# Optimization experiments

Measured on AMD Instinct MI355X. Metric: run time of the kernel, lower is better.

## Reference

```python
import jax, jax.numpy as jnp
import numpy as np

B, N, E, C, ND, MID, OUT = 4, 16384, 131072, 128, 3, 128, 128


def setup_inputs() -> dict:
    key = jax.random.key(0)
    ks = jax.random.split(key, 11)
    f = jax.random.normal(ks[0], (B, C, N), dtype=jnp.float32)
    nodes = jax.random.normal(ks[1], (B, N, ND), dtype=jnp.float32)
    node_weights = jax.random.uniform(ks[2], (B, N, 1), dtype=jnp.float32)  # positive quadrature weights
    edges_index = jax.random.randint(ks[3], (B, E, 2), 0, N)
    edge_gradient_weights = jax.random.normal(ks[4], (B, E, ND), dtype=jnp.float32) * 0.1
    mlp_w1 = jax.random.normal(ks[5], (MID, ND * C), dtype=jnp.float32) * 0.02
    mlp_b1 = jnp.zeros((MID,), dtype=jnp.float32)
    mlp_w2 = jax.random.normal(ks[6], (OUT, MID), dtype=jnp.float32) * 0.02
    mlp_b2 = jnp.zeros((OUT,), dtype=jnp.float32)
    L = jax.random.normal(ks[7], (ND, ND), dtype=jnp.float32) * 0.1  # Cholesky factor (scaled for non-degenerate exp)
    chol_bias = jnp.zeros((ND,), dtype=jnp.float32)
    return dict(f=f, nodes=nodes, node_weights=node_weights, edges_index=edges_index,
                edge_gradient_weights=edge_gradient_weights, mlp_w1=mlp_w1, mlp_b1=mlp_b1,
                mlp_w2=mlp_w2, mlp_b2=mlp_b2, L=L, chol_bias=chol_bias)


def reference(f, nodes, node_weights, edges_index, edge_gradient_weights,
              mlp_w1, mlp_b1, mlp_w2, mlp_b2, L, chol_bias):
    b, c, n = f.shape
    nd = edge_gradient_weights.shape[-1]
    bidx = jnp.arange(b)[:, None]
    src_g = edges_index[..., 0]
    tgt_g = edges_index[..., 1]

    # ---- compute_gradient: gather f[src]-f[tgt], weight by edge_gradient_weights, scatter-add to target ----
    fT = f.transpose(0, 2, 1)  # (B,N,C)
    df = jnp.take_along_axis(fT, src_g[..., None], axis=1) - jnp.take_along_axis(fT, tgt_g[..., None], axis=1)  # (B,E,C)
    msg = (df[:, :, :, None] * edge_gradient_weights[:, :, None, :]).reshape(b, df.shape[1], c * nd)  # 'bed,bec->becd'
    grad = jnp.zeros((b, n, c * nd), f.dtype).at[bidx, tgt_g].add(msg)
    g = grad.transpose(0, 2, 1)  # (B, C*nd, N)

    # ---- pointwise MLP over channel dim (Conv1d k=1 -> GELU -> Conv1d k=1) ----
    h = jnp.einsum('mk,bkn->bmn', mlp_w1, g) + mlp_b1[None, :, None]
    h = jax.nn.gelu(h, approximate=False)
    h = jnp.einsum('om,bmn->bon', mlp_w2, h) + mlp_b2[None, :, None]
    fo = h.transpose(0, 2, 1)  # (B,N,OUT)
    o = fo.shape[-1]

    # ---- Gaussian edge kernel via Cholesky PSD form, with self-edges appended ----
    self_e = jnp.broadcast_to(jnp.arange(n)[None, :], (b, n))
    src = jnp.concatenate([src_g, self_e], axis=-1)
    tgt = jnp.concatenate([tgt_g, self_e], axis=-1)
    f_src = jnp.take_along_axis(fo, src[..., None], axis=1)  # (B,E+N,OUT)
    d = jnp.take_along_axis(nodes, src[..., None], axis=1) - jnp.take_along_axis(nodes, tgt[..., None], axis=1)  # (B,E+N,nd)
    Sigma = L @ L.T  # positive semi-definite inverse covariance
    dS = d @ Sigma.T + chol_bias  # F.linear
    w_src = jnp.take_along_axis(node_weights, src[..., None], axis=1)[..., 0]  # (B,E+N)
    kernel = w_src * jnp.exp(-jnp.einsum('bed,bed->be', d, dS))

    # ---- scatter-add normalization and aggregation ----
    inv = 1.0 / jnp.zeros((b, n), f.dtype).at[bidx, tgt].add(kernel)
    out = jnp.zeros((b, n, o), f.dtype).at[bidx, tgt].add(f_src * kernel[..., None]) * inv[..., None]
    return out.transpose(0, 2, 1)  # (B,OUT,N)
```

## Files before the change

### kernel.cpp

```cpp
#include <hip/hip_runtime.h>
#include <hip/hip_bf16.h>

static constexpr int B   = 4;
static constexpr int N   = 16384;
static constexpr int E   = 131072;
static constexpr int C   = 128;
static constexpr int ND  = 3;
static constexpr int MID = 128;
static constexpr int OUT = 128;
static constexpr int K1  = C * ND;
static constexpr int NT  = 32;
static constexpr int K1P = 392;

typedef __attribute__((ext_vector_type(8))) short bf16x8;
typedef __attribute__((ext_vector_type(4))) float f32x4;

__device__ __forceinline__ ushort f2bf(float x) {
    union { float f; unsigned u; } v; v.f = x;
    return (ushort)((v.u + 0x7fffu + ((v.u >> 16) & 1u)) >> 16);
}
__device__ __forceinline__ float bf2f(ushort u) {
    union { unsigned u; float f; } v; v.u = (unsigned)u << 16;
    return v.f;
}

__global__ void k_prep(const float* __restrict__ W1, const float* __restrict__ W2,
                       const float* __restrict__ L, ushort* __restrict__ W1p,
                       ushort* __restrict__ W2p, float* __restrict__ Sig) {
    int gid = blockIdx.x * 256 + threadIdx.x;
    for (int i = gid; i < 8 * 12 * 64 * 8; i += 64 * 256) {
        int j = i & 7, l = (i >> 3) & 63, t = (i >> 9) % 12, nt = (i >> 9) / 12;
        int n = nt * 16 + (l & 15);
        int k = t * 32 + ((l >> 4) & 3) * 8 + j;
        W1p[i] = f2bf(W1[n * K1 + k]);
    }
    for (int i = gid; i < 8 * 4 * 64 * 8; i += 64 * 256) {
        int j = i & 7, l = (i >> 3) & 63, t = (i >> 9) % 4, nt = (i >> 9) / 4;
        int n = nt * 16 + (l & 15);
        int k = t * 32 + ((l >> 4) & 3) * 8 + j;
        W2p[i] = f2bf(W2[n * MID + k]);
    }
    if (gid < 9) {
        int i = gid / 3, j = gid % 3;
        Sig[gid] = L[i * 3 + 0] * L[j * 3 + 0] + L[i * 3 + 1] * L[j * 3 + 1] +
                   L[i * 3 + 2] * L[j * 3 + 2];
    }
}

__global__ void k_transpose(const float* __restrict__ f, ushort* __restrict__ fT) {
    __shared__ float tile[32][33];
    int b = blockIdx.z;
    int n0 = blockIdx.x * 32, c0 = blockIdx.y * 32;
    const float* fb = f + (size_t)b * C * N;
    ushort* fTb = fT + (size_t)b * N * C;
    int tx = threadIdx.x, ty = threadIdx.y;
    #pragma unroll
    for (int i = 0; i < 32; i += 8)
        tile[ty + i][tx] = fb[(size_t)(c0 + ty + i) * N + n0 + tx];
    __syncthreads();
    #pragma unroll
    for (int i = 0; i < 32; i += 8)
        fTb[(size_t)(n0 + ty + i) * C + c0 + tx] = f2bf(tile[tx][ty + i]);
}

__global__ void k_count(const int2* __restrict__ ei2, int* __restrict__ deg) {
    int idx = blockIdx.x * 256 + threadIdx.x;
    int b = idx >> 17;
    int tgt = ei2[idx].y;
    atomicAdd(&deg[b * N + tgt], 1);
}

__global__ void k_scan1(const int4* __restrict__ degv, int* __restrict__ rowptr,
                        int* __restrict__ bsum) {
    __shared__ int s[256];
    int blk = blockIdx.x, t = threadIdx.x;
    int4 d = degv[blk * 256 + t];
    s[t] = d.x + d.y + d.z + d.w;
    __syncthreads();
    for (int off = 1; off < 256; off <<= 1) {
        int v = s[t];
        int u = (t >= off) ? s[t - off] : 0;
        __syncthreads();
        s[t] = v + u;
        __syncthreads();
    }
    int excl = (t == 0) ? 0 : s[t - 1];
    if (t == 255) bsum[blk] = s[255];
    int4 w;
    w.x = excl;
    w.y = excl + d.x;
    w.z = w.y + d.y;
    w.w = w.z + d.z;
    ((int4*)rowptr)[blk * 256 + t] = w;
}

__global__ void k_scan2(int* __restrict__ bsum, int* __restrict__ rowptr) {
    __shared__ int s[64];
    int t = threadIdx.x;
    s[t] = bsum[t];
    __syncthreads();
    for (int off = 1; off < 64; off <<= 1) {
        int v = s[t];
        int u = (t >= off) ? s[t - off] : 0;
        __syncthreads();
        s[t] = v + u;
        __syncthreads();
    }
    bsum[t] = (t == 0) ? 0 : s[t - 1];
    if (t == 63) rowptr[B * N] = s[63];
}

__global__ void k_scan3(int4* __restrict__ rowv, const int* __restrict__ bsum) {
    int i = blockIdx.x * 256 + threadIdx.x;
    int add = bsum[i >> 8];
    int4 v = rowv[i];
    v.x += add; v.y += add; v.z += add; v.w += add;
    rowv[i] = v;
}

__global__ void k_fill_perm(const int2* __restrict__ ei2,
                            const int* __restrict__ rowptr,
                            int* __restrict__ cursor, int* __restrict__ perm) {
    int idx = blockIdx.x * 256 + threadIdx.x;
    int b = idx >> 17;
    int tgt = ei2[idx].y;
    int bn = b * N + tgt;
    int pos = atomicAdd(&cursor[bn], 1);
    perm[rowptr[bn] + pos] = idx;
}

__global__ void k_fill_expand(const int* __restrict__ perm,
                              const int2* __restrict__ ei2,
                              const float* __restrict__ egw,
                              const float* __restrict__ nodes,
                              const float* __restrict__ nw,
                              const float* __restrict__ Sig,
                              const float* __restrict__ cb,
                              float4* __restrict__ egwp, float2* __restrict__ ka2) {
    int o = blockIdx.x * 256 + threadIdx.x;
    int idx = perm[o];
    int b = idx >> 17;
    int2 e = ei2[idx];
    int src = e.x, tgt = e.y;
    const float* w = egw + (size_t)idx * ND;
    egwp[o] = make_float4(w[0], w[1], w[2], __int_as_float(src));
    const float* ns = nodes + ((size_t)b * N + src) * ND;
    const float* nt = nodes + ((size_t)b * N + tgt) * ND;
    float d0 = ns[0] - nt[0], d1 = ns[1] - nt[1], d2 = ns[2] - nt[2];
    float q = d0 * (Sig[0] * d0 + Sig[1] * d1 + Sig[2] * d2) +
              d1 * (Sig[3] * d0 + Sig[4] * d1 + Sig[5] * d2) +
              d2 * (Sig[6] * d0 + Sig[7] * d1 + Sig[8] * d2) +
              d0 * cb[0] + d1 * cb[1] + d2 * cb[2];
    ka2[o] = make_float2(nw[(size_t)b * N + src] * expf(-q), __int_as_float(src));
}

#define EDGE_FMA(W, U)                                                         \
    {                                                                          \
        float dx = bf2f(U.x) - ft.x, dy = bf2f(U.y) - ft.y,                    \
              dz = bf2f(U.z) - ft.z, dw = bf2f(U.w) - ft.w;                    \
        a0.x = fmaf(dx, W.x, a0.x); a0.y = fmaf(dy, W.x, a0.y);                \
        a0.z = fmaf(dz, W.x, a0.z); a0.w = fmaf(dw, W.x, a0.w);                \
        a1.x = fmaf(dx, W.y, a1.x); a1.y = fmaf(dy, W.y, a1.y);                \
        a1.z = fmaf(dz, W.y, a1.z); a1.w = fmaf(dw, W.y, a1.w);                \
        a2.x = fmaf(dx, W.z, a2.x); a2.y = fmaf(dy, W.z, a2.y);                \
        a2.z = fmaf(dz, W.z, a2.z); a2.w = fmaf(dw, W.z, a2.w);                \
    }

__global__ __launch_bounds__(512, 5) void k_grad_mlp(
    const ushort* __restrict__ fT, const int* __restrict__ rowptr,
    const float4* __restrict__ egwp, const ushort* __restrict__ W1p,
    const float* __restrict__ b1, const ushort* __restrict__ W2p,
    const float* __restrict__ b2, ushort* __restrict__ fo) {
    __shared__ ushort g_s[NT][K1P];
    int tid = threadIdx.x;
    int n0 = blockIdx.x * NT;

    {
        int cg = tid & 31, s = tid >> 5;
        int cg4 = cg * 4;
        for (int jj = 0; jj < NT; jj += 16) {
            int j = jj + s;
            int n = n0 + j;
            const ushort* fTb = fT + (size_t)(n >> 14) * N * C;
            float4 ft;
            {
                ushort4 u = *(const ushort4*)(fT + (size_t)n * C + cg4);
                ft = make_float4(bf2f(u.x), bf2f(u.y), bf2f(u.z), bf2f(u.w));
            }
            int base = rowptr[n], cnt = rowptr[n + 1] - base;
            float4 a0 = make_float4(0.f, 0.f, 0.f, 0.f), a1 = a0, a2 = a0;
            int i = 0;
            for (; i + 4 <= cnt; i += 4) {
                float4 w0 = egwp[base + i];
                float4 w1 = egwp[base + i + 1];
                float4 w2 = egwp[base + i + 2];
                float4 w3 = egwp[base + i + 3];
                ushort4 u0 = *(const ushort4*)(fTb + (size_t)__float_as_int(w0.w) * C + cg4);
                ushort4 u1 = *(const ushort4*)(fTb + (size_t)__float_as_int(w1.w) * C + cg4);
                ushort4 u2 = *(const ushort4*)(fTb + (size_t)__float_as_int(w2.w) * C + cg4);
                ushort4 u3 = *(const ushort4*)(fTb + (size_t)__float_as_int(w3.w) * C + cg4);
                EDGE_FMA(w0, u0);
                EDGE_FMA(w1, u1);
                EDGE_FMA(w2, u2);
                EDGE_FMA(w3, u3);
            }
            for (; i < cnt; ++i) {
                float4 w0 = egwp[base + i];
                ushort4 u0 = *(const ushort4*)(fTb + (size_t)__float_as_int(w0.w) * C + cg4);
                EDGE_FMA(w0, u0);
            }
            unsigned p0 = (unsigned)f2bf(a0.x) | ((unsigned)f2bf(a1.x) << 16);
            unsigned p1 = (unsigned)f2bf(a2.x) | ((unsigned)f2bf(a0.y) << 16);
            unsigned p2 = (unsigned)f2bf(a1.y) | ((unsigned)f2bf(a2.y) << 16);
            unsigned p3 = (unsigned)f2bf(a0.z) | ((unsigned)f2bf(a1.z) << 16);
            unsigned p4 = (unsigned)f2bf(a2.z) | ((unsigned)f2bf(a0.w) << 16);
            unsigned p5 = (unsigned)f2bf(a1.w) | ((unsigned)f2bf(a2.w) << 16);
            uint2* dst = (uint2*)&g_s[j][cg * 12];
            dst[0] = make_uint2(p0, p1);
            dst[1] = make_uint2(p2, p3);
            dst[2] = make_uint2(p4, p5);
        }
    }
    __syncthreads();

    int wv = tid >> 6, ln = tid & 63, lr = ln & 15, lh = ln >> 4;
    int mt = wv & 1, nh = wv >> 1;
    bf16x8 a[12];
    {
        const ushort* grow = &g_s[mt * 16 + lr][0];
        #pragma unroll
        for (int t = 0; t < 12; ++t)
            a[t] = *(const bf16x8*)(grow + t * 32 + lh * 8);
    }
    __syncthreads();

    ushort(*h_s)[136] = (ushort(*)[136]) & g_s[0][0];
    const bf16x8* W1f = (const bf16x8*)W1p;
    #pragma unroll
    for (int q = 0; q < 2; ++q) {
        int nt = nh * 2 + q;
        float bb = b1[nt * 16 + lr];
        f32x4 c = {bb, bb, bb, bb};
        #pragma unroll
        for (int t = 0; t < 12; ++t)
            c = __builtin_amdgcn_mfma_f32_16x16x32_bf16(
                a[t], W1f[(nt * 12 + t) * 64 + ln], c, 0, 0, 0);
        #pragma unroll
        for (int r = 0; r < 4; ++r) {
            float x = c[r];
            x = 0.5f * x * (1.0f + erff(x * 0.70710678118654752f));
            h_s[mt * 16 + lh * 4 + r][nt * 16 + lr] = f2bf(x);
        }
    }
    __syncthreads();

    bf16x8 a2[4];
    {
        const ushort* hrow = &h_s[mt * 16 + lr][0];
        #pragma unroll
        for (int t = 0; t < 4; ++t)
            a2[t] = *(const bf16x8*)(hrow + t * 32 + lh * 8);
    }
    const bf16x8* W2f = (const bf16x8*)W2p;
    #pragma unroll
    for (int q = 0; q < 2; ++q) {
        int nt = nh * 2 + q;
        float bb = b2[nt * 16 + lr];
        f32x4 c = {bb, bb, bb, bb};
        #pragma unroll
        for (int t = 0; t < 4; ++t)
            c = __builtin_amdgcn_mfma_f32_16x16x32_bf16(
                a2[t], W2f[(nt * 4 + t) * 64 + ln], c, 0, 0, 0);
        #pragma unroll
        for (int r = 0; r < 4; ++r)
            fo[(size_t)(n0 + mt * 16 + lh * 4 + r) * OUT + nt * 16 + lr] = f2bf(c[r]);
    }
}

#define AGG_FMA(K, U)                                                          \
    {                                                                          \
        o.x = fmaf(bf2f(U.x), K.x, o.x); o.y = fmaf(bf2f(U.y), K.x, o.y);      \
        o.z = fmaf(bf2f(U.z), K.x, o.z); o.w = fmaf(bf2f(U.w), K.x, o.w);      \
        den += K.x;                                                            \
    }

__global__ __launch_bounds__(512, 5) void k_agg_t(const ushort* __restrict__ fo,
                                                  const float* __restrict__ nw,
                                                  const int* __restrict__ rowptr,
                                                  const float2* __restrict__ ka2,
                                                  float* __restrict__ out) {
    __shared__ float t[OUT][65];
    int tid = threadIdx.x;
    int cg4 = (tid & 31) * 4;
    int s = tid >> 5;
    int n0 = blockIdx.x * 64;
    int b = n0 >> 14, ncol0 = n0 & (N - 1);
    const ushort* fob = fo + (size_t)b * N * OUT;
    for (int g = 0; g < 4; ++g) {
        int nl = g * 16 + s;
        int n = n0 + nl;
        int base = rowptr[n], cnt = rowptr[n + 1] - base;
        float4 o = make_float4(0.f, 0.f, 0.f, 0.f);
        float den = 0.f;
        int i = 0;
        for (; i + 4 <= cnt; i += 4) {
            float2 k0 = ka2[base + i];
            float2 k1 = ka2[base + i + 1];
            float2 k2 = ka2[base + i + 2];
            float2 k3 = ka2[base + i + 3];
            ushort4 u0 = *(const ushort4*)(fob + (size_t)__float_as_int(k0.y) * OUT + cg4);
            ushort4 u1 = *(const ushort4*)(fob + (size_t)__float_as_int(k1.y) * OUT + cg4);
            ushort4 u2 = *(const ushort4*)(fob + (size_t)__float_as_int(k2.y) * OUT + cg4);
            ushort4 u3 = *(const ushort4*)(fob + (size_t)__float_as_int(k3.y) * OUT + cg4);
            AGG_FMA(k0, u0);
            AGG_FMA(k1, u1);
            AGG_FMA(k2, u2);
            AGG_FMA(k3, u3);
        }
        for (; i < cnt; ++i) {
            float2 k0 = ka2[base + i];
            ushort4 u0 = *(const ushort4*)(fob + (size_t)__float_as_int(k0.y) * OUT + cg4);
            AGG_FMA(k0, u0);
        }
        float wn = nw[n];
        ushort4 uf = *(const ushort4*)(fo + (size_t)n * OUT + cg4);
        float inv = 1.f / (den + wn);
        t[cg4 + 0][nl] = (o.x + bf2f(uf.x) * wn) * inv;
        t[cg4 + 1][nl] = (o.y + bf2f(uf.y) * wn) * inv;
        t[cg4 + 2][nl] = (o.z + bf2f(uf.z) * wn) * inv;
        t[cg4 + 3][nl] = (o.w + bf2f(uf.w) * wn) * inv;
    }
    __syncthreads();
    #pragma unroll
    for (int i = 0; i < 16; ++i) {
        int idx = tid + i * 512;
        int o = idx >> 6, nl = idx & 63;
        out[((size_t)b * OUT + o) * N + ncol0 + nl] = t[o][nl];
    }
}

extern "C" void kernel_launch(void* const* d_in, const int* in_sizes, int n_in,
                              void* d_out, int out_size, void* d_ws, size_t ws_size,
                              hipStream_t stream) {
    const float* f     = (const float*)d_in[0];
    const float* nodes = (const float*)d_in[1];
    const float* nw    = (const float*)d_in[2];
    const int*   ei    = (const int*)d_in[3];
    const float* egw   = (const float*)d_in[4];
    const float* W1    = (const float*)d_in[5];
    const float* b1    = (const float*)d_in[6];
    const float* W2    = (const float*)d_in[7];
    const float* b2    = (const float*)d_in[8];
    const float* L     = (const float*)d_in[9];
    const float* cb    = (const float*)d_in[10];
    float* out = (float*)d_out;

    char* ws = (char*)d_ws;
    auto alloc = [&](size_t bytes) {
        void* p = ws;
        ws += (bytes + 255) & ~(size_t)255;
        return p;
    };
    ushort* fT     = (ushort*)alloc((size_t)B * N * C * 2);
    ushort* fo     = (ushort*)alloc((size_t)B * N * OUT * 2);
    ushort* W1p    = (ushort*)alloc((size_t)MID * K1 * 2);
    ushort* W2p    = (ushort*)alloc((size_t)OUT * MID * 2);
    float*  Sig    = (float*)alloc(16 * 4);
    int*    deg    = (int*)alloc((size_t)B * N * 4);
    int*    cursor = (int*)alloc((size_t)B * N * 4);
    int*    rowptr = (int*)alloc(((size_t)B * N + 4) * 4);
    int*    bsum   = (int*)alloc(64 * 4);
    int*    perm   = (int*)alloc((size_t)B * E * 4);
    float4* egwp   = (float4*)alloc((size_t)B * E * 16);
    float2* ka2    = (float2*)alloc((size_t)B * E * 8);

    hipMemsetAsync(deg, 0, (size_t)B * N * 4, stream);
    hipMemsetAsync(cursor, 0, (size_t)B * N * 4, stream);

    k_prep<<<64, 256, 0, stream>>>(W1, W2, L, W1p, W2p, Sig);
    k_transpose<<<dim3(N / 32, C / 32, B), dim3(32, 8), 0, stream>>>(f, fT);
    k_count<<<(B * E) / 256, 256, 0, stream>>>((const int2*)ei, deg);
    k_scan1<<<64, 256, 0, stream>>>((const int4*)deg, rowptr, bsum);
    k_scan2<<<1, 64, 0, stream>>>(bsum, rowptr);
    k_scan3<<<64, 256, 0, stream>>>((int4*)rowptr, bsum);
    k_fill_perm<<<(B * E) / 256, 256, 0, stream>>>((const int2*)ei, rowptr, cursor,
                                                   perm);
    k_fill_expand<<<(B * E) / 256, 256, 0, stream>>>(perm, (const int2*)ei, egw,
                                                     nodes, nw, Sig, cb, egwp, ka2);
    k_grad_mlp<<<(B * N) / NT, 512, 0, stream>>>(fT, rowptr, egwp, W1p, b1, W2p,
                                                 b2, fo);
    k_agg_t<<<(B * N) / 64, 512, 0, stream>>>(fo, nw, rowptr, ka2, out);
}
```

Before: 171.6 us.

## Fuse front kernels, factor gradient subtraction, and widen gather loads to 8 channels

Merges the weight-prep, transpose and degree-count kernels into one launch and replaces the two memsets with one covering deg and cursor, which sit next to each other. The gradient gather now sums f[src]*w and subtracts f[tgt]*sum(w) once per node instead of per edge. It also processes one node per 16 threads using 8-channel (16-byte) loads. The aggregation kernel is likewise widened to 8 channels per thread. The intent is to cut launch overhead, per-edge arithmetic and load instruction count, at the cost of more registers and a slightly different rounding order.

```diff
diff --git a/kernel.cpp b/kernel.cpp
--- a/kernel.cpp
+++ b/kernel.cpp
@@ -13,6 +13,7 @@
 static constexpr int K1P = 392;
 
 typedef __attribute__((ext_vector_type(8))) short bf16x8;
+typedef __attribute__((ext_vector_type(8))) unsigned short ushort8v;
 typedef __attribute__((ext_vector_type(4))) float f32x4;
 
 __device__ __forceinline__ ushort f2bf(float x) {
@@ -24,50 +25,52 @@
     return v.f;
 }
 
-__global__ void k_prep(const float* __restrict__ W1, const float* __restrict__ W2,
-                       const float* __restrict__ L, ushort* __restrict__ W1p,
-                       ushort* __restrict__ W2p, float* __restrict__ Sig) {
-    int gid = blockIdx.x * 256 + threadIdx.x;
-    for (int i = gid; i < 8 * 12 * 64 * 8; i += 64 * 256) {
-        int j = i & 7, l = (i >> 3) & 63, t = (i >> 9) % 12, nt = (i >> 9) / 12;
-        int n = nt * 16 + (l & 15);
-        int k = t * 32 + ((l >> 4) & 3) * 8 + j;
-        W1p[i] = f2bf(W1[n * K1 + k]);
-    }
-    for (int i = gid; i < 8 * 4 * 64 * 8; i += 64 * 256) {
-        int j = i & 7, l = (i >> 3) & 63, t = (i >> 9) % 4, nt = (i >> 9) / 4;
-        int n = nt * 16 + (l & 15);
-        int k = t * 32 + ((l >> 4) & 3) * 8 + j;
-        W2p[i] = f2bf(W2[n * MID + k]);
-    }
-    if (gid < 9) {
-        int i = gid / 3, j = gid % 3;
-        Sig[gid] = L[i * 3 + 0] * L[j * 3 + 0] + L[i * 3 + 1] * L[j * 3 + 1] +
-                   L[i * 3 + 2] * L[j * 3 + 2];
-    }
-}
-
-__global__ void k_transpose(const float* __restrict__ f, ushort* __restrict__ fT) {
+__global__ void k_front(const float* __restrict__ f, ushort* __restrict__ fT,
+                        const int2* __restrict__ ei2, int* __restrict__ deg,
+                        const float* __restrict__ W1, const float* __restrict__ W2,
+                        const float* __restrict__ L, ushort* __restrict__ W1p,
+                        ushort* __restrict__ W2p, float* __restrict__ Sig) {
     __shared__ float tile[32][33];
-    int b = blockIdx.z;
-    int n0 = blockIdx.x * 32, c0 = blockIdx.y * 32;
-    const float* fb = f + (size_t)b * C * N;
-    ushort* fTb = fT + (size_t)b * N * C;
-    int tx = threadIdx.x, ty = threadIdx.y;
-    #pragma unroll
-    for (int i = 0; i < 32; i += 8)
-        tile[ty + i][tx] = fb[(size_t)(c0 + ty + i) * N + n0 + tx];
-    __syncthreads();
-    #pragma unroll
-    for (int i = 0; i < 32; i += 8)
-        fTb[(size_t)(n0 + ty + i) * C + c0 + tx] = f2bf(tile[tx][ty + i]);
-}
-
-__global__ void k_count(const int2* __restrict__ ei2, int* __restrict__ deg) {
-    int idx = blockIdx.x * 256 + threadIdx.x;
-    int b = idx >> 17;
-    int tgt = ei2[idx].y;
-    atomicAdd(&deg[b * N + tgt], 1);
+    int bid = blockIdx.x, tid = threadIdx.x;
+    if (bid < 8192) {
+        int bx = bid & 511, by = (bid >> 9) & 3, b = bid >> 11;
+        int n0 = bx * 32, c0 = by * 32;
+        const float* fb = f + (size_t)b * C * N;
+        ushort* fTb = fT + (size_t)b * N * C;
+        int tx = tid & 31, ty = tid >> 5;
+        #pragma unroll
+        for (int i = 0; i < 32; i += 8)
+            tile[ty + i][tx] = fb[(size_t)(c0 + ty + i) * N + n0 + tx];
+        __syncthreads();
+        #pragma unroll
+        for (int i = 0; i < 32; i += 8)
+            fTb[(size_t)(n0 + ty + i) * C + c0 + tx] = f2bf(tile[tx][ty + i]);
+    } else if (bid < 10240) {
+        int idx = (bid - 8192) * 256 + tid;
+        int b = idx >> 17;
+        int tgt = ei2[idx].y;
+        atomicAdd(&deg[b * N + tgt], 1);
+    } else {
+        int gid = (bid - 10240) * 256 + tid;
+        for (int i = gid; i < 8 * 12 * 64 * 8; i += 64 * 256) {
+            int j = i & 7, l = (i >> 3) & 63, t = (i >> 9) % 12, nt = (i >> 9) / 12;
+            int n = nt * 16 + (l & 15);
+            int k = t * 32 + ((l >> 4) & 3) * 8 + j;
+            W1p[i] = f2bf(W1[n * K1 + k]);
+        }
+        {
+            int i = gid;
+            int j = i & 7, l = (i >> 3) & 63, t = (i >> 9) % 4, nt = (i >> 9) / 4;
+            int n = nt * 16 + (l & 15);
+            int k = t * 32 + ((l >> 4) & 3) * 8 + j;
+            W2p[i] = f2bf(W2[n * MID + k]);
+        }
+        if (gid < 9) {
+            int i = gid / 3, j = gid % 3;
+            Sig[gid] = L[i * 3 + 0] * L[j * 3 + 0] + L[i * 3 + 1] * L[j * 3 + 1] +
+                       L[i * 3 + 2] * L[j * 3 + 2];
+        }
+    }
 }
 
 __global__ void k_scan1(const int4* __restrict__ degv, int* __restrict__ rowptr,
@@ -154,16 +157,15 @@
     ka2[o] = make_float2(nw[(size_t)b * N + src] * expf(-q), __int_as_float(src));
 }
 
-#define EDGE_FMA(W, U)                                                         \
+#define GEDGE(W, U)                                                            \
     {                                                                          \
-        float dx = bf2f(U.x) - ft.x, dy = bf2f(U.y) - ft.y,                    \
-              dz = bf2f(U.z) - ft.z, dw = bf2f(U.w) - ft.w;                    \
-        a0.x = fmaf(dx, W.x, a0.x); a0.y = fmaf(dy, W.x, a0.y);                \
-        a0.z = fmaf(dz, W.x, a0.z); a0.w = fmaf(dw, W.x, a0.w);                \
-        a1.x = fmaf(dx, W.y, a1.x); a1.y = fmaf(dy, W.y, a1.y);                \
-        a1.z = fmaf(dz, W.y, a1.z); a1.w = fmaf(dw, W.y, a1.w);                \
-        a2.x = fmaf(dx, W.z, a2.x); a2.y = fmaf(dy, W.z, a2.y);                \
-        a2.z = fmaf(dz, W.z, a2.z); a2.w = fmaf(dw, W.z, a2.w);                \
+        sw0 += W.x; sw1 += W.y; sw2 += W.z;                                    \
+        _Pragma("unroll") for (int u = 0; u < 8; ++u) {                        \
+            float fv = bf2f((ushort)U[u]);                                     \
+            a0[u] = fmaf(fv, W.x, a0[u]);                                      \
+            a1[u] = fmaf(fv, W.y, a1[u]);                                      \
+            a2[u] = fmaf(fv, W.z, a2[u]);                                      \
+        }                                                                      \
     }
 
 __global__ __launch_bounds__(512, 5) void k_grad_mlp(
@@ -176,50 +178,47 @@
     int n0 = blockIdx.x * NT;
 
     {
-        int cg = tid & 31, s = tid >> 5;
-        int cg4 = cg * 4;
-        for (int jj = 0; jj < NT; jj += 16) {
-            int j = jj + s;
-            int n = n0 + j;
-            const ushort* fTb = fT + (size_t)(n >> 14) * N * C;
-            float4 ft;
-            {
-                ushort4 u = *(const ushort4*)(fT + (size_t)n * C + cg4);
-                ft = make_float4(bf2f(u.x), bf2f(u.y), bf2f(u.z), bf2f(u.w));
-            }
-            int base = rowptr[n], cnt = rowptr[n + 1] - base;
-            float4 a0 = make_float4(0.f, 0.f, 0.f, 0.f), a1 = a0, a2 = a0;
-            int i = 0;
-            for (; i + 4 <= cnt; i += 4) {
-                float4 w0 = egwp[base + i];
-                float4 w1 = egwp[base + i + 1];
-                float4 w2 = egwp[base + i + 2];
-                float4 w3 = egwp[base + i + 3];
-                ushort4 u0 = *(const ushort4*)(fTb + (size_t)__float_as_int(w0.w) * C + cg4);
-                ushort4 u1 = *(const ushort4*)(fTb + (size_t)__float_as_int(w1.w) * C + cg4);
-                ushort4 u2 = *(const ushort4*)(fTb + (size_t)__float_as_int(w2.w) * C + cg4);
-                ushort4 u3 = *(const ushort4*)(fTb + (size_t)__float_as_int(w3.w) * C + cg4);
-                EDGE_FMA(w0, u0);
-                EDGE_FMA(w1, u1);
-                EDGE_FMA(w2, u2);
-                EDGE_FMA(w3, u3);
-            }
-            for (; i < cnt; ++i) {
-                float4 w0 = egwp[base + i];
-                ushort4 u0 = *(const ushort4*)(fTb + (size_t)__float_as_int(w0.w) * C + cg4);
-                EDGE_FMA(w0, u0);
-            }
-            unsigned p0 = (unsigned)f2bf(a0.x) | ((unsigned)f2bf(a1.x) << 16);
-            unsigned p1 = (unsigned)f2bf(a2.x) | ((unsigned)f2bf(a0.y) << 16);
-            unsigned p2 = (unsigned)f2bf(a1.y) | ((unsigned)f2bf(a2.y) << 16);
-            unsigned p3 = (unsigned)f2bf(a0.z) | ((unsigned)f2bf(a1.z) << 16);
-            unsigned p4 = (unsigned)f2bf(a2.z) | ((unsigned)f2bf(a0.w) << 16);
-            unsigned p5 = (unsigned)f2bf(a1.w) | ((unsigned)f2bf(a2.w) << 16);
-            uint2* dst = (uint2*)&g_s[j][cg * 12];
-            dst[0] = make_uint2(p0, p1);
-            dst[1] = make_uint2(p2, p3);
-            dst[2] = make_uint2(p4, p5);
-        }
+        int cg = tid & 15, s = tid >> 4;
+        int cg8 = cg * 8;
+        int n = n0 + s;
+        const ushort* fTb = fT + (size_t)(n >> 14) * N * C;
+        ushort8v ftr = *(const ushort8v*)(fT + (size_t)n * C + cg8);
+        int base = rowptr[n], cnt = rowptr[n + 1] - base;
+        float a0[8], a1[8], a2[8];
+        #pragma unroll
+        for (int u = 0; u < 8; ++u) { a0[u] = 0.f; a1[u] = 0.f; a2[u] = 0.f; }
+        float sw0 = 0.f, sw1 = 0.f, sw2 = 0.f;
+        int i = 0;
+        for (; i + 2 <= cnt; i += 2) {
+            float4 w0 = egwp[base + i];
+            float4 w1 = egwp[base + i + 1];
+            ushort8v u0 = *(const ushort8v*)(fTb + (size_t)__float_as_int(w0.w) * C + cg8);
+            ushort8v u1 = *(const ushort8v*)(fTb + (size_t)__float_as_int(w1.w) * C + cg8);
+            GEDGE(w0, u0);
+            GEDGE(w1, u1);
+        }
+        if (i < cnt) {
+            float4 w0 = egwp[base + i];
+            ushort8v u0 = *(const ushort8v*)(fTb + (size_t)__float_as_int(w0.w) * C + cg8);
+            GEDGE(w0, u0);
+        }
+        unsigned p[12];
+        #pragma unroll
+        for (int u = 0; u < 4; ++u) {
+            float ge0 = a0[2 * u] - bf2f((ushort)ftr[2 * u]) * sw0;
+            float ge1 = a1[2 * u] - bf2f((ushort)ftr[2 * u]) * sw1;
+            float ge2 = a2[2 * u] - bf2f((ushort)ftr[2 * u]) * sw2;
+            float go0 = a0[2 * u + 1] - bf2f((ushort)ftr[2 * u + 1]) * sw0;
+            float go1 = a1[2 * u + 1] - bf2f((ushort)ftr[2 * u + 1]) * sw1;
+            float go2 = a2[2 * u + 1] - bf2f((ushort)ftr[2 * u + 1]) * sw2;
+            p[3 * u + 0] = (unsigned)f2bf(ge0) | ((unsigned)f2bf(ge1) << 16);
+            p[3 * u + 1] = (unsigned)f2bf(ge2) | ((unsigned)f2bf(go0) << 16);
+            p[3 * u + 2] = (unsigned)f2bf(go1) | ((unsigned)f2bf(go2) << 16);
+        }
+        uint4* dst = (uint4*)&g_s[s][cg * 24];
+        dst[0] = make_uint4(p[0], p[1], p[2], p[3]);
+        dst[1] = make_uint4(p[4], p[5], p[6], p[7]);
+        dst[2] = make_uint4(p[8], p[9], p[10], p[11]);
     }
     __syncthreads();
 
@@ -277,11 +276,11 @@
     }
 }
 
-#define AGG_FMA(K, U)                                                          \
+#define AGG8(K, U)                                                             \
     {                                                                          \
-        o.x = fmaf(bf2f(U.x), K.x, o.x); o.y = fmaf(bf2f(U.y), K.x, o.y);      \
-        o.z = fmaf(bf2f(U.z), K.x, o.z); o.w = fmaf(bf2f(U.w), K.x, o.w);      \
         den += K.x;                                                            \
+        _Pragma("unroll") for (int u = 0; u < 8; ++u)                          \
+            o8[u] = fmaf(bf2f((ushort)U[u]), K.x, o8[u]);                      \
     }
 
 __global__ __launch_bounds__(512, 5) void k_agg_t(const ushort* __restrict__ fo,
@@ -291,16 +290,19 @@
                                                   float* __restrict__ out) {
     __shared__ float t[OUT][65];
     int tid = threadIdx.x;
-    int cg4 = (tid & 31) * 4;
-    int s = tid >> 5;
+    int cg = tid & 15, s = tid >> 4;
+    int cg8 = cg * 8;
     int n0 = blockIdx.x * 64;
     int b = n0 >> 14, ncol0 = n0 & (N - 1);
     const ushort* fob = fo + (size_t)b * N * OUT;
-    for (int g = 0; g < 4; ++g) {
-        int nl = g * 16 + s;
+    #pragma unroll
+    for (int g = 0; g < 2; ++g) {
+        int nl = g * 32 + s;
         int n = n0 + nl;
         int base = rowptr[n], cnt = rowptr[n + 1] - base;
-        float4 o = make_float4(0.f, 0.f, 0.f, 0.f);
+        float o8[8];
+        #pragma unroll
+        for (int u = 0; u < 8; ++u) o8[u] = 0.f;
         float den = 0.f;
         int i = 0;
         for (; i + 4 <= cnt; i += 4) {
@@ -308,27 +310,26 @@
             float2 k1 = ka2[base + i + 1];
             float2 k2 = ka2[base + i + 2];
             float2 k3 = ka2[base + i + 3];
-            ushort4 u0 = *(const ushort4*)(fob + (size_t)__float_as_int(k0.y) * OUT + cg4);
-            ushort4 u1 = *(const ushort4*)(fob + (size_t)__float_as_int(k1.y) * OUT + cg4);
-            ushort4 u2 = *(const ushort4*)(fob + (size_t)__float_as_int(k2.y) * OUT + cg4);
-            ushort4 u3 = *(const ushort4*)(fob + (size_t)__float_as_int(k3.y) * OUT + cg4);
-            AGG_FMA(k0, u0);
-            AGG_FMA(k1, u1);
-            AGG_FMA(k2, u2);
-            AGG_FMA(k3, u3);
+            ushort8v u0 = *(const ushort8v*)(fob + (size_t)__float_as_int(k0.y) * OUT + cg8);
+            ushort8v u1 = *(const ushort8v*)(fob + (size_t)__float_as_int(k1.y) * OUT + cg8);
+            ushort8v u2 = *(const ushort8v*)(fob + (size_t)__float_as_int(k2.y) * OUT + cg8);
+            ushort8v u3 = *(const ushort8v*)(fob + (size_t)__float_as_int(k3.y) * OUT + cg8);
+            AGG8(k0, u0);
+            AGG8(k1, u1);
+            AGG8(k2, u2);
+            AGG8(k3, u3);
         }
         for (; i < cnt; ++i) {
             float2 k0 = ka2[base + i];
-            ushort4 u0 = *(const ushort4*)(fob + (size_t)__float_as_int(k0.y) * OUT + cg4);
-            AGG_FMA(k0, u0);
+            ushort8v u0 = *(const ushort8v*)(fob + (size_t)__float_as_int(k0.y) * OUT + cg8);
+            AGG8(k0, u0);
         }
         float wn = nw[n];
-        ushort4 uf = *(const ushort4*)(fo + (size_t)n * OUT + cg4);
+        ushort8v uf = *(const ushort8v*)(fo + (size_t)n * OUT + cg8);
         float inv = 1.f / (den + wn);
-        t[cg4 + 0][nl] = (o.x + bf2f(uf.x) * wn) * inv;
-        t[cg4 + 1][nl] = (o.y + bf2f(uf.y) * wn) * inv;
-        t[cg4 + 2][nl] = (o.z + bf2f(uf.z) * wn) * inv;
-        t[cg4 + 3][nl] = (o.w + bf2f(uf.w) * wn) * inv;
+        #pragma unroll
+        for (int u = 0; u < 8; ++u)
+            t[cg8 + u][nl] = (o8[u] + bf2f((ushort)uf[u]) * wn) * inv;
     }
     __syncthreads();
     #pragma unroll
@@ -374,12 +375,10 @@
     float4* egwp   = (float4*)alloc((size_t)B * E * 16);
     float2* ka2    = (float2*)alloc((size_t)B * E * 8);
 
-    hipMemsetAsync(deg, 0, (size_t)B * N * 4, stream);
-    hipMemsetAsync(cursor, 0, (size_t)B * N * 4, stream);
-
-    k_prep<<<64, 256, 0, stream>>>(W1, W2, L, W1p, W2p, Sig);
-    k_transpose<<<dim3(N / 32, C / 32, B), dim3(32, 8), 0, stream>>>(f, fT);
-    k_count<<<(B * E) / 256, 256, 0, stream>>>((const int2*)ei, deg);
+    hipMemsetAsync(deg, 0, (size_t)B * N * 4 * 2, stream);
+
+    k_front<<<10304, 256, 0, stream>>>(f, fT, (const int2*)ei, deg, W1, W2, L,
+                                       W1p, W2p, Sig);
     k_scan1<<<64, 256, 0, stream>>>((const int4*)deg, rowptr, bsum);
     k_scan2<<<1, 64, 0, stream>>>(bsum, rowptr);
     k_scan3<<<64, 256, 0, stream>>>((int4*)rowptr, bsum);
```

Measured after the change: 155.9 us. 1.1x faster.

## Fuse front-end kernels, merge memsets, swizzle blocks per XCD, deepen edge unroll

Applied to the files above, without the earlier changes.

Merges the weight-pack, transpose and degree-count kernels into one launch split by block-index ranges. The two memsets become a single one over the contiguous deg/cursor buffers. Remaps block indices in the gradient-MLP and aggregation kernels so each of the 8 XCDs gets a contiguous node range, aiming at better L2 locality. Unrolls the edge gather to 8 loads in flight. This cuts launch overhead and gather latency, at the cost of more register pressure and some branch divergence in the fused kernel.

```diff
diff --git a/kernel.cpp b/kernel.cpp
--- a/kernel.cpp
+++ b/kernel.cpp
@@ -24,50 +24,52 @@
     return v.f;
 }
 
-__global__ void k_prep(const float* __restrict__ W1, const float* __restrict__ W2,
-                       const float* __restrict__ L, ushort* __restrict__ W1p,
-                       ushort* __restrict__ W2p, float* __restrict__ Sig) {
-    int gid = blockIdx.x * 256 + threadIdx.x;
-    for (int i = gid; i < 8 * 12 * 64 * 8; i += 64 * 256) {
-        int j = i & 7, l = (i >> 3) & 63, t = (i >> 9) % 12, nt = (i >> 9) / 12;
-        int n = nt * 16 + (l & 15);
-        int k = t * 32 + ((l >> 4) & 3) * 8 + j;
-        W1p[i] = f2bf(W1[n * K1 + k]);
-    }
-    for (int i = gid; i < 8 * 4 * 64 * 8; i += 64 * 256) {
-        int j = i & 7, l = (i >> 3) & 63, t = (i >> 9) % 4, nt = (i >> 9) / 4;
-        int n = nt * 16 + (l & 15);
-        int k = t * 32 + ((l >> 4) & 3) * 8 + j;
-        W2p[i] = f2bf(W2[n * MID + k]);
-    }
-    if (gid < 9) {
-        int i = gid / 3, j = gid % 3;
-        Sig[gid] = L[i * 3 + 0] * L[j * 3 + 0] + L[i * 3 + 1] * L[j * 3 + 1] +
-                   L[i * 3 + 2] * L[j * 3 + 2];
-    }
-}
-
-__global__ void k_transpose(const float* __restrict__ f, ushort* __restrict__ fT) {
+__global__ void k_front(const float* __restrict__ f, ushort* __restrict__ fT,
+                        const int2* __restrict__ ei2, int* __restrict__ deg,
+                        const float* __restrict__ W1, const float* __restrict__ W2,
+                        const float* __restrict__ L, ushort* __restrict__ W1p,
+                        ushort* __restrict__ W2p, float* __restrict__ Sig) {
     __shared__ float tile[32][33];
-    int b = blockIdx.z;
-    int n0 = blockIdx.x * 32, c0 = blockIdx.y * 32;
-    const float* fb = f + (size_t)b * C * N;
-    ushort* fTb = fT + (size_t)b * N * C;
-    int tx = threadIdx.x, ty = threadIdx.y;
-    #pragma unroll
-    for (int i = 0; i < 32; i += 8)
-        tile[ty + i][tx] = fb[(size_t)(c0 + ty + i) * N + n0 + tx];
-    __syncthreads();
-    #pragma unroll
-    for (int i = 0; i < 32; i += 8)
-        fTb[(size_t)(n0 + ty + i) * C + c0 + tx] = f2bf(tile[tx][ty + i]);
-}
-
-__global__ void k_count(const int2* __restrict__ ei2, int* __restrict__ deg) {
-    int idx = blockIdx.x * 256 + threadIdx.x;
-    int b = idx >> 17;
-    int tgt = ei2[idx].y;
-    atomicAdd(&deg[b * N + tgt], 1);
+    int bid = blockIdx.x, tid = threadIdx.x;
+    if (bid < 8192) {
+        int bx = bid & 511, by = (bid >> 9) & 3, b = bid >> 11;
+        int n0 = bx * 32, c0 = by * 32;
+        const float* fb = f + (size_t)b * C * N;
+        ushort* fTb = fT + (size_t)b * N * C;
+        int tx = tid & 31, ty = tid >> 5;
+        #pragma unroll
+        for (int i = 0; i < 32; i += 8)
+            tile[ty + i][tx] = fb[(size_t)(c0 + ty + i) * N + n0 + tx];
+        __syncthreads();
+        #pragma unroll
+        for (int i = 0; i < 32; i += 8)
+            fTb[(size_t)(n0 + ty + i) * C + c0 + tx] = f2bf(tile[tx][ty + i]);
+    } else if (bid < 10240) {
+        int idx = (bid - 8192) * 256 + tid;
+        int b = idx >> 17;
+        int tgt = ei2[idx].y;
+        atomicAdd(&deg[b * N + tgt], 1);
+    } else {
+        int gid = (bid - 10240) * 256 + tid;
+        for (int i = gid; i < 8 * 12 * 64 * 8; i += 64 * 256) {
+            int j = i & 7, l = (i >> 3) & 63, t = (i >> 9) % 12, nt = (i >> 9) / 12;
+            int n = nt * 16 + (l & 15);
+            int k = t * 32 + ((l >> 4) & 3) * 8 + j;
+            W1p[i] = f2bf(W1[n * K1 + k]);
+        }
+        {
+            int i = gid;
+            int j = i & 7, l = (i >> 3) & 63, t = (i >> 9) % 4, nt = (i >> 9) / 4;
+            int n = nt * 16 + (l & 15);
+            int k = t * 32 + ((l >> 4) & 3) * 8 + j;
+            W2p[i] = f2bf(W2[n * MID + k]);
+        }
+        if (gid < 9) {
+            int i = gid / 3, j = gid % 3;
+            Sig[gid] = L[i * 3 + 0] * L[j * 3 + 0] + L[i * 3 + 1] * L[j * 3 + 1] +
+                       L[i * 3 + 2] * L[j * 3 + 2];
+        }
+    }
 }
 
 __global__ void k_scan1(const int4* __restrict__ degv, int* __restrict__ rowptr,
@@ -166,6 +168,10 @@
         a2.z = fmaf(dz, W.z, a2.z); a2.w = fmaf(dw, W.z, a2.w);                \
     }
 
+#define EDGE_LOAD(K)                                                           \
+    float4 w##K = egwp[base + i + K];                                          \
+    ushort4 u##K = *(const ushort4*)(fTb + (size_t)__float_as_int(w##K.w) * C + cg4);
+
 __global__ __launch_bounds__(512, 5) void k_grad_mlp(
     const ushort* __restrict__ fT, const int* __restrict__ rowptr,
     const float4* __restrict__ egwp, const ushort* __restrict__ W1p,
@@ -173,7 +179,9 @@
     const float* __restrict__ b2, ushort* __restrict__ fo) {
     __shared__ ushort g_s[NT][K1P];
     int tid = threadIdx.x;
-    int n0 = blockIdx.x * NT;
+    int bid = blockIdx.x;
+    int swz = (bid & 7) * ((B * N / NT) >> 3) + (bid >> 3);
+    int n0 = swz * NT;
 
     {
         int cg = tid & 31, s = tid >> 5;
@@ -190,23 +198,21 @@
             int base = rowptr[n], cnt = rowptr[n + 1] - base;
             float4 a0 = make_float4(0.f, 0.f, 0.f, 0.f), a1 = a0, a2 = a0;
             int i = 0;
+            for (; i + 8 <= cnt; i += 8) {
+                EDGE_LOAD(0); EDGE_LOAD(1); EDGE_LOAD(2); EDGE_LOAD(3);
+                EDGE_LOAD(4); EDGE_LOAD(5); EDGE_LOAD(6); EDGE_LOAD(7);
+                EDGE_FMA(w0, u0); EDGE_FMA(w1, u1);
+                EDGE_FMA(w2, u2); EDGE_FMA(w3, u3);
+                EDGE_FMA(w4, u4); EDGE_FMA(w5, u5);
+                EDGE_FMA(w6, u6); EDGE_FMA(w7, u7);
+            }
             for (; i + 4 <= cnt; i += 4) {
-                float4 w0 = egwp[base + i];
-                float4 w1 = egwp[base + i + 1];
-                float4 w2 = egwp[base + i + 2];
-                float4 w3 = egwp[base + i + 3];
-                ushort4 u0 = *(const ushort4*)(fTb + (size_t)__float_as_int(w0.w) * C + cg4);
-                ushort4 u1 = *(const ushort4*)(fTb + (size_t)__float_as_int(w1.w) * C + cg4);
-                ushort4 u2 = *(const ushort4*)(fTb + (size_t)__float_as_int(w2.w) * C + cg4);
-                ushort4 u3 = *(const ushort4*)(fTb + (size_t)__float_as_int(w3.w) * C + cg4);
-                EDGE_FMA(w0, u0);
-                EDGE_FMA(w1, u1);
-                EDGE_FMA(w2, u2);
-                EDGE_FMA(w3, u3);
+                EDGE_LOAD(0); EDGE_LOAD(1); EDGE_LOAD(2); EDGE_LOAD(3);
+                EDGE_FMA(w0, u0); EDGE_FMA(w1, u1);
+                EDGE_FMA(w2, u2); EDGE_FMA(w3, u3);
             }
             for (; i < cnt; ++i) {
-                float4 w0 = egwp[base + i];
-                ushort4 u0 = *(const ushort4*)(fTb + (size_t)__float_as_int(w0.w) * C + cg4);
+                EDGE_LOAD(0);
                 EDGE_FMA(w0, u0);
             }
             unsigned p0 = (unsigned)f2bf(a0.x) | ((unsigned)f2bf(a1.x) << 16);
@@ -293,9 +299,12 @@
     int tid = threadIdx.x;
     int cg4 = (tid & 31) * 4;
     int s = tid >> 5;
-    int n0 = blockIdx.x * 64;
+    int bid = blockIdx.x;
+    int swz = (bid & 7) * ((B * N / 64) >> 3) + (bid >> 3);
+    int n0 = swz * 64;
     int b = n0 >> 14, ncol0 = n0 & (N - 1);
     const ushort* fob = fo + (size_t)b * N * OUT;
+    #pragma unroll
     for (int g = 0; g < 4; ++g) {
         int nl = g * 16 + s;
         int n = n0 + nl;
@@ -374,12 +383,10 @@
     float4* egwp   = (float4*)alloc((size_t)B * E * 16);
     float2* ka2    = (float2*)alloc((size_t)B * E * 8);
 
-    hipMemsetAsync(deg, 0, (size_t)B * N * 4, stream);
-    hipMemsetAsync(cursor, 0, (size_t)B * N * 4, stream);
-
-    k_prep<<<64, 256, 0, stream>>>(W1, W2, L, W1p, W2p, Sig);
-    k_transpose<<<dim3(N / 32, C / 32, B), dim3(32, 8), 0, stream>>>(f, fT);
-    k_count<<<(B * E) / 256, 256, 0, stream>>>((const int2*)ei, deg);
+    hipMemsetAsync(deg, 0, (size_t)B * N * 4 * 2, stream);
+
+    k_front<<<10304, 256, 0, stream>>>(f, fT, (const int2*)ei, deg, W1, W2, L,
+                                       W1p, W2p, Sig);
     k_scan1<<<64, 256, 0, stream>>>((const int4*)deg, rowptr, bsum);
     k_scan2<<<1, 64, 0, stream>>>(bsum, rowptr);
     k_scan3<<<64, 256, 0, stream>>>((int4*)rowptr, bsum);
```

After: 171.0 us. No clear change (-0.3%).
